# Performance work log

Hardware: AMD Instinct MI355X
Metric: run time of the kernel (lower is better)

The kernel has to match this reference:

```python
import jax, jax.numpy as jnp
import numpy as np


def setup_inputs() -> dict:
    key = jax.random.key(0)
    k1, k2, k3, k4, k5 = jax.random.split(key, 5)
    B, S, D, H, L = 32, 2048, 512, 32, 2
    inp = jax.random.normal(k1, (B, S, D), dtype=jnp.float32)
    mask = jax.random.randint(k2, (B, S), 0, 2) > 0  # bool [B,S]
    projector = jax.random.normal(k3, (D, H), dtype=jnp.float32) * 0.05
    hidden = jax.random.normal(k4, (L - 1, H, H), dtype=jnp.float32) * 0.05
    evaluator = jax.random.normal(k5, (H, 1), dtype=jnp.float32) * 0.05
    return {"inp": inp, "mask": mask, "projector": projector,
            "hidden": hidden, "evaluator": evaluator}


def reference(inp, mask, projector, hidden, evaluator):
    act = jax.nn.sigmoid
    scale = jnp.asarray(projector.shape[-1], inp.dtype) ** 0.5  # sqrt(hidden_dim)
    m = mask.astype(inp.dtype)[..., None]          # [B,S,1]
    x = inp * m                                     # masked inputs (inp *= mask)
    w = act(jnp.einsum('bsd,dh->bsh', x, projector) / scale)
    for i in range(hidden.shape[0]):                # n_layers - 1 hidden matmuls
        w = act(jnp.einsum('bsh,hk->bsk', w, hidden[i]) / scale)
    w = act(jnp.einsum('bsh,ho->bso', w, evaluator) / scale)  # [B,S,1]
    w = jax.nn.softmax(w, axis=-2)                  # softmax over sequence axis
    w = w * m
    w = w / (jnp.sum(w, axis=1, keepdims=True) + 1e-12)
    return jnp.sum(w * x, axis=1)                   # [B,D]
```

## Files before the change

kernel.cpp:

```cpp
#include <hip/hip_runtime.h>

#define B_   32
#define S_   2048
#define D_   512
#define H_   32
#define BS_  (B_*S_)
#define INV_SCALE 0.17677669529663689f


typedef short  s16x8 __attribute__((ext_vector_type(8)));
typedef float  f32x4 __attribute__((ext_vector_type(4)));

__device__ __forceinline__ float sigmoidf_(float x) {
    return 1.0f / (1.0f + __expf(-x));
}

__device__ __forceinline__ unsigned short f2bf(float f) {
    unsigned u = __float_as_uint(f);
    u += 0x7fffu + ((u >> 16) & 1u);
    return (unsigned short)(u >> 16);
}

__global__ void kTransposeBf(const float* __restrict__ P, unsigned short* __restrict__ PTbf) {
    int o = blockIdx.x * 256 + threadIdx.x;
    int j = o >> 9, d = o & 511;
    PTbf[o] = f2bf(P[d * H_ + j]);
}

#define XST 520

__global__ __launch_bounds__(256) void kFused(
        const float* __restrict__ inp, const int* __restrict__ mask,
        const unsigned short* __restrict__ PTbf, const float* __restrict__ hd,
        const float* __restrict__ ev,
        float* __restrict__ partial, float2* __restrict__ zdm) {
    __shared__ unsigned short xs[32 * XST];
    __shared__ float w0f[32 * 33];
    __shared__ float w1f[32 * 33];
    __shared__ float cs[32];

    const int tid = threadIdx.x;
    const int blk = blockIdx.x;
    const int rowBase = blk * 32;

    const float4* g = (const float4*)inp + (size_t)rowBase * 128;
    float4 tmp[16];
    #pragma unroll
    for (int i = 0; i < 16; ++i)
        tmp[i] = g[i * 256 + tid];
    #pragma unroll
    for (int i = 0; i < 16; ++i) {
        int fi = i * 256 + tid;
        int row = fi >> 7, kq = fi & 127;
        ushort4 u;
        u.x = f2bf(tmp[i].x); u.y = f2bf(tmp[i].y);
        u.z = f2bf(tmp[i].z); u.w = f2bf(tmp[i].w);
        *(ushort4*)(xs + row * XST + kq * 4) = u;
    }
    __syncthreads();

    const int wave = tid >> 6, lane = tid & 63;
    const int rt = wave & 1, ct = wave >> 1;
    const int m = lane & 15, quad = lane >> 4;

    const unsigned short* arow = xs + (rt * 16 + m) * XST + quad * 8;
    const unsigned short* brow = PTbf + (size_t)(ct * 16 + m) * 512 + quad * 8;

    f32x4 acc = {0.f, 0.f, 0.f, 0.f};
    #pragma unroll
    for (int ks = 0; ks < 16; ++ks) {
        s16x8 a = *(const s16x8*)(arow + ks * 32);
        s16x8 b = *(const s16x8*)(brow + ks * 32);
        acc = __builtin_amdgcn_mfma_f32_16x16x32_bf16(a, b, acc, 0, 0, 0);
    }

    #pragma unroll
    for (int r = 0; r < 4; ++r) {
        int rowL = rt * 16 + quad * 4 + r;
        float mr = (mask[rowBase + rowL] != 0) ? 1.0f : 0.0f;
        w0f[rowL * 33 + ct * 16 + m] = sigmoidf_(mr * acc[r] * INV_SCALE);
    }
    __syncthreads();

    {
        const int k = tid & 31, slot = tid >> 5;
        #pragma unroll
        for (int t = 0; t < 4; ++t) {
            int row = slot + 8 * t;
            float s = 0.f;
            #pragma unroll
            for (int j = 0; j < 32; ++j)
                s = fmaf(w0f[row * 33 + j], hd[j * 32 + k], s);
            w1f[row * 33 + k] = sigmoidf_(s * INV_SCALE);
        }
    }
    __syncthreads();

    if (tid < 64) {
        float e = 0.f, mm = 0.f;
        if (tid < 32) {
            float s = 0.f;
            #pragma unroll
            for (int k = 0; k < 32; ++k)
                s = fmaf(w1f[tid * 33 + k], ev[k], s);
            float val = sigmoidf_(s * INV_SCALE);
            e  = __expf(val);
            mm = (mask[rowBase + tid] != 0) ? 1.0f : 0.0f;
            cs[tid] = mm * e;
        }
        float z = e, dm = mm * e;
        #pragma unroll
        for (int o = 32; o > 0; o >>= 1) {
            z  += __shfl_down(z, o);
            dm += __shfl_down(dm, o);
        }
        if (tid == 0) zdm[blk] = make_float2(z, dm);
    }
    __syncthreads();

    float a0 = 0.f, a1 = 0.f;
    #pragma unroll 8
    for (int row = 0; row < 32; ++row) {
        unsigned u = *(const unsigned*)(xs + row * XST + 2 * tid);
        float x0 = __uint_as_float(u << 16);
        float x1 = __uint_as_float(u & 0xffff0000u);
        float c = cs[row];
        a0 = fmaf(c, x0, a0);
        a1 = fmaf(c, x1, a1);
    }
    ((float2*)(partial + (size_t)blk * 512))[tid] = make_float2(a0, a1);
}

__global__ __launch_bounds__(256) void kReduce(
        const float* __restrict__ partial, const float2* __restrict__ zdm,
        float* __restrict__ out) {
    const int b = blockIdx.x, tid = threadIdx.x;
    __shared__ float sInv;

    if (tid < 64) {
        float2 p = zdm[b * 64 + tid];
        float z = p.x, dm = p.y;
        #pragma unroll
        for (int o = 32; o > 0; o >>= 1) {
            z  += __shfl_down(z, o);
            dm += __shfl_down(dm, o);
        }
        if (tid == 0) sInv = 1.0f / (dm + 1e-12f * z);
    }
    __syncthreads();

    const float2* pp = (const float2*)partial + (size_t)b * 64 * 256 + tid;
    float a0 = 0.f, b0 = 0.f, a1 = 0.f, b1 = 0.f;
    float a2 = 0.f, b2 = 0.f, a3 = 0.f, b3 = 0.f;
    #pragma unroll
    for (int i = 0; i < 64; i += 4) {
        float2 p0 = pp[(size_t)(i + 0) * 256];
        float2 p1 = pp[(size_t)(i + 1) * 256];
        float2 p2 = pp[(size_t)(i + 2) * 256];
        float2 p3 = pp[(size_t)(i + 3) * 256];
        a0 += p0.x; b0 += p0.y; a1 += p1.x; b1 += p1.y;
        a2 += p2.x; b2 += p2.y; a3 += p3.x; b3 += p3.y;
    }
    const float inv = sInv;
    float2 r;
    r.x = ((a0 + a1) + (a2 + a3)) * inv;
    r.y = ((b0 + b1) + (b2 + b3)) * inv;
    ((float2*)out)[b * 256 + tid] = r;
}

extern "C" void kernel_launch(void* const* d_in, const int* in_sizes, int n_in,
                              void* d_out, int out_size, void* d_ws, size_t ws_size,
                              hipStream_t stream) {
    const float* inp  = (const float*)d_in[0];
    const int*   mask = (const int*)d_in[1];
    const float* proj = (const float*)d_in[2];
    const float* hid  = (const float*)d_in[3];
    const float* ev   = (const float*)d_in[4];
    float* out = (float*)d_out;

    unsigned short* PTbf = (unsigned short*)d_ws;
    float2* zdm     = (float2*)((char*)d_ws + 32768);
    float*  partial = (float*)((char*)d_ws + 49152);

    kTransposeBf<<<64, 256, 0, stream>>>(proj, PTbf);
    kFused      <<<BS_ / 32, 256, 0, stream>>>(inp, mask, PTbf, hid, ev, partial, zdm);
    kReduce     <<<B_, 256, 0, stream>>>(partial, zdm, out);
}
```

Measured before the change: 221.6 us.

## Halve fused tile to 16 rows and pool from fp32 registers

Measured after the change: 236.9 us. 6.9% more time.

```diff
diff --git a/kernel.cpp b/kernel.cpp
--- a/kernel.cpp
+++ b/kernel.cpp
@@ -29,41 +29,39 @@
 
 #define XST 520
 
-__global__ __launch_bounds__(256) void kFused(
+__global__ __launch_bounds__(128) void kFused(
         const float* __restrict__ inp, const int* __restrict__ mask,
         const unsigned short* __restrict__ PTbf, const float* __restrict__ hd,
         const float* __restrict__ ev,
         float* __restrict__ partial, float2* __restrict__ zdm) {
-    __shared__ unsigned short xs[32 * XST];
-    __shared__ float w0f[32 * 33];
-    __shared__ float w1f[32 * 33];
-    __shared__ float cs[32];
+    __shared__ unsigned short xs[16 * XST];
+    __shared__ float w0f[16 * 33];
+    __shared__ float w1f[16 * 33];
+    __shared__ float cs[16];
 
     const int tid = threadIdx.x;
     const int blk = blockIdx.x;
-    const int rowBase = blk * 32;
+    const int rowBase = blk * 16;
 
     const float4* g = (const float4*)inp + (size_t)rowBase * 128;
     float4 tmp[16];
     #pragma unroll
     for (int i = 0; i < 16; ++i)
-        tmp[i] = g[i * 256 + tid];
+        tmp[i] = g[i * 128 + tid];
     #pragma unroll
     for (int i = 0; i < 16; ++i) {
-        int fi = i * 256 + tid;
-        int row = fi >> 7, kq = fi & 127;
         ushort4 u;
         u.x = f2bf(tmp[i].x); u.y = f2bf(tmp[i].y);
         u.z = f2bf(tmp[i].z); u.w = f2bf(tmp[i].w);
-        *(ushort4*)(xs + row * XST + kq * 4) = u;
+        *(ushort4*)(xs + i * XST + tid * 4) = u;
     }
     __syncthreads();
 
     const int wave = tid >> 6, lane = tid & 63;
-    const int rt = wave & 1, ct = wave >> 1;
+    const int ct = wave;
     const int m = lane & 15, quad = lane >> 4;
 
-    const unsigned short* arow = xs + (rt * 16 + m) * XST + quad * 8;
+    const unsigned short* arow = xs + m * XST + quad * 8;
     const unsigned short* brow = PTbf + (size_t)(ct * 16 + m) * 512 + quad * 8;
 
     f32x4 acc = {0.f, 0.f, 0.f, 0.f};
@@ -76,7 +74,7 @@
 
     #pragma unroll
     for (int r = 0; r < 4; ++r) {
-        int rowL = rt * 16 + quad * 4 + r;
+        int rowL = quad * 4 + r;
         float mr = (mask[rowBase + rowL] != 0) ? 1.0f : 0.0f;
         w0f[rowL * 33 + ct * 16 + m] = sigmoidf_(mr * acc[r] * INV_SCALE);
     }
@@ -86,7 +84,7 @@
         const int k = tid & 31, slot = tid >> 5;
         #pragma unroll
         for (int t = 0; t < 4; ++t) {
-            int row = slot + 8 * t;
+            int row = slot + 4 * t;
             float s = 0.f;
             #pragma unroll
             for (int j = 0; j < 32; ++j)
@@ -98,7 +96,7 @@
 
     if (tid < 64) {
         float e = 0.f, mm = 0.f;
-        if (tid < 32) {
+        if (tid < 16) {
             float s = 0.f;
             #pragma unroll
             for (int k = 0; k < 32; ++k)
@@ -118,28 +116,31 @@
     }
     __syncthreads();
 
-    float a0 = 0.f, a1 = 0.f;
-    #pragma unroll 8
-    for (int row = 0; row < 32; ++row) {
-        unsigned u = *(const unsigned*)(xs + row * XST + 2 * tid);
-        float x0 = __uint_as_float(u << 16);
-        float x1 = __uint_as_float(u & 0xffff0000u);
-        float c = cs[row];
-        a0 = fmaf(c, x0, a0);
-        a1 = fmaf(c, x1, a1);
-    }
-    ((float2*)(partial + (size_t)blk * 512))[tid] = make_float2(a0, a1);
+    float4 a0 = make_float4(0.f, 0.f, 0.f, 0.f);
+    #pragma unroll
+    for (int i = 0; i < 16; ++i) {
+        float c = cs[i];
+        a0.x = fmaf(c, tmp[i].x, a0.x);
+        a0.y = fmaf(c, tmp[i].y, a0.y);
+        a0.z = fmaf(c, tmp[i].z, a0.z);
+        a0.w = fmaf(c, tmp[i].w, a0.w);
+    }
+    ((float4*)partial)[(size_t)blk * 128 + tid] = a0;
 }
 
 __global__ __launch_bounds__(256) void kReduce(
         const float* __restrict__ partial, const float2* __restrict__ zdm,
         float* __restrict__ out) {
-    const int b = blockIdx.x, tid = threadIdx.x;
+    const int b = blockIdx.x >> 3, dc = blockIdx.x & 7;
+    const int tid = threadIdx.x;
+    const int sg = tid >> 4, dl = tid & 15;
     __shared__ float sInv;
+    __shared__ float4 red[256];
 
     if (tid < 64) {
-        float2 p = zdm[b * 64 + tid];
-        float z = p.x, dm = p.y;
+        float2 p0 = zdm[b * 128 + tid];
+        float2 p1 = zdm[b * 128 + 64 + tid];
+        float z = p0.x + p1.x, dm = p0.y + p1.y;
         #pragma unroll
         for (int o = 32; o > 0; o >>= 1) {
             z  += __shfl_down(z, o);
@@ -147,25 +148,44 @@
         }
         if (tid == 0) sInv = 1.0f / (dm + 1e-12f * z);
     }
-    __syncthreads();
-
-    const float2* pp = (const float2*)partial + (size_t)b * 64 * 256 + tid;
-    float a0 = 0.f, b0 = 0.f, a1 = 0.f, b1 = 0.f;
-    float a2 = 0.f, b2 = 0.f, a3 = 0.f, b3 = 0.f;
-    #pragma unroll
-    for (int i = 0; i < 64; i += 4) {
-        float2 p0 = pp[(size_t)(i + 0) * 256];
-        float2 p1 = pp[(size_t)(i + 1) * 256];
-        float2 p2 = pp[(size_t)(i + 2) * 256];
-        float2 p3 = pp[(size_t)(i + 3) * 256];
-        a0 += p0.x; b0 += p0.y; a1 += p1.x; b1 += p1.y;
-        a2 += p2.x; b2 += p2.y; a3 += p3.x; b3 += p3.y;
-    }
-    const float inv = sInv;
-    float2 r;
-    r.x = ((a0 + a1) + (a2 + a3)) * inv;
-    r.y = ((b0 + b1) + (b2 + b3)) * inv;
-    ((float2*)out)[b * 256 + tid] = r;
+
+    const float4* pp = (const float4*)partial + (size_t)(b * 128) * 128 + dc * 16 + dl;
+    float4 a0 = make_float4(0,0,0,0), a1 = a0, a2 = a0, a3 = a0;
+    #pragma unroll
+    for (int i = 0; i < 8; i += 4) {
+        float4 p0 = pp[(size_t)(sg + (i + 0) * 16) * 128];
+        float4 p1 = pp[(size_t)(sg + (i + 1) * 16) * 128];
+        float4 p2 = pp[(size_t)(sg + (i + 2) * 16) * 128];
+        float4 p3 = pp[(size_t)(sg + (i + 3) * 16) * 128];
+        a0.x += p0.x; a0.y += p0.y; a0.z += p0.z; a0.w += p0.w;
+        a1.x += p1.x; a1.y += p1.y; a1.z += p1.z; a1.w += p1.w;
+        a2.x += p2.x; a2.y += p2.y; a2.z += p2.z; a2.w += p2.w;
+        a3.x += p3.x; a3.y += p3.y; a3.z += p3.z; a3.w += p3.w;
+    }
+    float4 a;
+    a.x = (a0.x + a1.x) + (a2.x + a3.x);
+    a.y = (a0.y + a1.y) + (a2.y + a3.y);
+    a.z = (a0.z + a1.z) + (a2.z + a3.z);
+    a.w = (a0.w + a1.w) + (a2.w + a3.w);
+    red[tid] = a;
+    __syncthreads();
+
+    #pragma unroll
+    for (int h = 8; h >= 1; h >>= 1) {
+        if (sg < h) {
+            float4 p = red[(sg + h) * 16 + dl];
+            float4 q = red[tid];
+            q.x += p.x; q.y += p.y; q.z += p.z; q.w += p.w;
+            red[tid] = q;
+        }
+        __syncthreads();
+    }
+    if (tid < 16) {
+        const float inv = sInv;
+        float4 r = red[tid];
+        r.x *= inv; r.y *= inv; r.z *= inv; r.w *= inv;
+        ((float4*)out)[b * 128 + dc * 16 + tid] = r;
+    }
 }
 
 extern "C" void kernel_launch(void* const* d_in, const int* in_sizes, int n_in,
@@ -180,9 +200,9 @@
 
     unsigned short* PTbf = (unsigned short*)d_ws;
     float2* zdm     = (float2*)((char*)d_ws + 32768);
-    float*  partial = (float*)((char*)d_ws + 49152);
+    float*  partial = (float*)((char*)d_ws + 65536);
 
     kTransposeBf<<<64, 256, 0, stream>>>(proj, PTbf);
-    kFused      <<<BS_ / 32, 256, 0, stream>>>(inp, mask, PTbf, hid, ev, partial, zdm);
-    kReduce     <<<B_, 256, 0, stream>>>(partial, zdm, out);
-}
+    kFused      <<<BS_ / 16, 128, 0, stream>>>(inp, mask, PTbf, hid, ev, partial, zdm);
+    kReduce     <<<B_ * 8, 256, 0, stream>>>(partial, zdm, out);
+}
```
